# Optimization experiments

Measured on AMD Instinct MI355X. Metric: run time of the kernel, lower is better.

Reference implementation:

```python
import jax, jax.numpy as jnp
import numpy as np

D_IN = 1024
D_OUT = 1024
SEQ = 4096


def setup_inputs() -> dict:
    key = jax.random.key(0)
    kx, kq, kk, kv = jax.random.split(key, 4)
    s = 1.0 / np.sqrt(D_IN)
    return {
        "x": jax.random.normal(kx, (SEQ, D_IN), dtype=jnp.float32),
        # torch Linear weights: shape [d_out, d_in], y = x @ W.T
        "Wq": jax.random.uniform(kq, (D_OUT, D_IN), jnp.float32, -s, s),
        "Wk": jax.random.uniform(kk, (D_OUT, D_IN), jnp.float32, -s, s),
        "Wv": jax.random.uniform(kv, (D_OUT, D_IN), jnp.float32, -s, s),
    }


def reference(x, Wq, Wk, Wv):
    # QKV projections (no bias)
    q = x @ Wq.T  # [N, d_out]
    k = x @ Wk.T
    v = x @ Wv.T
    scale = 1.0 / jnp.sqrt(jnp.asarray(k.shape[-1], x.dtype))
    att = jax.nn.softmax((q @ k.T) * scale, axis=-1)  # [N, N]
    return att @ v  # [N, d_out]
```

## Files before the change

### kernel.cpp

```cpp
#include <hip/hip_runtime.h>
#include <hip/hip_bf16.h>
#include <math.h>

typedef __attribute__((ext_vector_type(8))) short short8;
typedef __attribute__((ext_vector_type(4))) float floatx4;

static __device__ __forceinline__ unsigned short f2bf(float f) {
    union { float f; unsigned int u; } a; a.f = f;
    unsigned int u = a.u;
    return (unsigned short)((u + 0x7FFFu + ((u >> 16) & 1u)) >> 16);
}
static __device__ __forceinline__ float bf2f(unsigned short h) {
    union { unsigned int u; float f; } a; a.u = ((unsigned int)h) << 16;
    return a.f;
}

static __device__ __forceinline__ void cvt8(const float* __restrict__ src,
                                            unsigned short* __restrict__ dst, int i) {
    float4 v0 = *(const float4*)(src + i);
    float4 v1 = *(const float4*)(src + i + 4);
    ushort4 o0, o1;
    o0.x = f2bf(v0.x); o0.y = f2bf(v0.y); o0.z = f2bf(v0.z); o0.w = f2bf(v0.w);
    o1.x = f2bf(v1.x); o1.y = f2bf(v1.y); o1.z = f2bf(v1.z); o1.w = f2bf(v1.w);
    *(ushort4*)(dst + i) = o0;
    *(ushort4*)(dst + i + 4) = o1;
}

struct CV { const float* x; unsigned short* xb;
            const float* W[3]; unsigned short* Wb[3]; float* l; };
__global__ __launch_bounds__(256)
void cvt_all(CV a) {
    int b = blockIdx.x, t = threadIdx.x;
    if (b < 2048) {
        cvt8(a.x, a.xb, (b * 256 + t) * 8);
    } else if (b < 3584) {
        int z  = (b - 2048) >> 9;
        int bb = (b - 2048) & 511;
        cvt8(a.W[z], a.Wb[z], (bb * 256 + t) * 8);
    } else {
        float4 zz = {0.f, 0.f, 0.f, 0.f};
        #pragma unroll
        for (int c = 0; c < 4; c++)
            *(float4*)(a.l + t * 16 + c * 4) = zz;
    }
}

#define DSR(dst, base, OFF)                                                    \
    asm volatile("ds_read_b128 %0, %1 offset:%2"                               \
                 : "=v"(dst) : "v"(base), "n"(OFF))
#define DSR4(arr, base, O)                                                     \
    do { DSR(arr[0], base, (O));        DSR(arr[1], base, (O) + 1024);         \
         DSR(arr[2], base, (O) + 2048); DSR(arr[3], base, (O) + 3072); } while (0)
#define LGKM(N) asm volatile("s_waitcnt lgkmcnt(" #N ")" ::: "memory")
#define SBAR()  asm volatile("s_barrier" ::: "memory")
#define SB0     __builtin_amdgcn_sched_barrier(0)

typedef __attribute__((address_space(3))) char* lds3p;

__device__ __forceinline__ void gemm256_core(
    const unsigned short* __restrict__ A, const unsigned short* __restrict__ B,
    int lda, int k_begin, int bm, int bn,
    unsigned short* lds, floatx4 (&acc)[8][4])
{
    const int t    = threadIdx.x;
    const int wave = t >> 6;
    const int lane = t & 63;
    const int wrow = wave >> 2;
    const int wcol = wave & 3;
    const int lm   = lane & 15;
    const int ce8  = (((lane >> 4) ^ ((lm >> 1) & 3)) << 3);

    const int srow = t >> 2;
    const int gsh  = (((t & 3) ^ ((srow >> 1) & 3)) << 3);
    const unsigned short* srcA = A + (size_t)(bm + srow) * lda + k_begin + gsh;
    const unsigned short* srcB = B + (size_t)(bn + srow) * lda + k_begin + gsh;
    const size_t rstep = (size_t)128 * lda;
    char* ldsc = (char*)lds;
    const int w1k = wave << 10;

    lds3p lp3 = (lds3p)lds;
    lds3p va = lp3 + (((wrow << 7) + lm) * 64 + (ce8 << 1));
    lds3p vb = lp3 + (65536 + ((wcol << 6) + lm) * 64 + (ce8 << 1));

#define STAGE(kind, kh, tau) do {                                              \
        int taue_ = (tau) >= 16 ? (tau) - 2 : (tau);   \
        int ko_ = (taue_ << 6) + ((kh) << 5);                                  \
        unsigned lo_ = ((kind) << 16) + (((tau) & 1) << 15) + ((kh) << 14) + w1k; \
        const unsigned short* s_ = ((kind) ? srcB : srcA) + ko_;               \
        __builtin_amdgcn_global_load_lds(                                      \
            (const __attribute__((address_space(1))) void*)s_,                 \
            (__attribute__((address_space(3))) void*)(ldsc + lo_), 16, 0, 0);  \
        __builtin_amdgcn_global_load_lds(                                      \
            (const __attribute__((address_space(1))) void*)(s_ + rstep),       \
            (__attribute__((address_space(3))) void*)(ldsc + lo_ + 8192), 16, 0, 0); \
    } while (0)

#define MF1(R, AV, BV)                                                         \
    do {                                                                       \
        acc[R][0] = __builtin_amdgcn_mfma_f32_16x16x32_bf16(AV, BV[0], acc[R][0], 0, 0, 0); \
        acc[R][1] = __builtin_amdgcn_mfma_f32_16x16x32_bf16(AV, BV[1], acc[R][1], 0, 0, 0); \
        acc[R][2] = __builtin_amdgcn_mfma_f32_16x16x32_bf16(AV, BV[2], acc[R][2], 0, 0, 0); \
        acc[R][3] = __builtin_amdgcn_mfma_f32_16x16x32_bf16(AV, BV[3], acc[R][3], 0, 0, 0); \
    } while (0)
#define MFMAG(R0, NA, BV)                                                      \
    do { MF1((R0) + 0, NA[0], BV); MF1((R0) + 1, NA[1], BV);                   \
         MF1((R0) + 2, NA[2], BV); MF1((R0) + 3, NA[3], BV); } while (0)

    STAGE(1, 0, 0); STAGE(0, 0, 0); STAGE(1, 1, 0); STAGE(0, 1, 0);
    STAGE(1, 0, 1); STAGE(0, 0, 1); STAGE(1, 1, 1);
    asm volatile("s_waitcnt vmcnt(6)" ::: "memory");
    SBAR();

    constexpr int DB = 32768, KH = 16384;
    short8 naA[4], naB[4], bA[4], bB[4];
    DSR4(naA, va, 0);
    DSR4(bA,  vb, 0);

#define FOURPH(PBc, PBn, TC)                                                   \
                         \
    DSR4(naB, va, (PBc) + 4096);                                               \
    STAGE(0, 1, (TC) + 1);                                                     \
    SBAR(); LGKM(4); SB0;                                                      \
    __builtin_amdgcn_s_setprio(1);                                             \
    MFMAG(0, naA, bA); SB0;                                                    \
    __builtin_amdgcn_s_setprio(0);                                             \
    SBAR();                                                                    \
         \
    DSR4(naA, va, (PBc) + KH);                                                 \
    DSR4(bB,  vb, (PBc) + KH);                                                 \
    STAGE(1, 0, (TC) + 2);                                                     \
    SBAR(); LGKM(8); SB0;                                                      \
    __builtin_amdgcn_s_setprio(1);                                             \
    MFMAG(4, naB, bA); SB0;                                                    \
    __builtin_amdgcn_s_setprio(0);                                             \
    SBAR();                                                                    \
                         \
    DSR4(naB, va, (PBc) + KH + 4096);                                          \
    STAGE(0, 0, (TC) + 2);                                                     \
    SBAR(); LGKM(4); SB0;                                                      \
    __builtin_amdgcn_s_setprio(1);                                             \
    MFMAG(0, naA, bB); SB0;                                                    \
    __builtin_amdgcn_s_setprio(0);                                             \
    SBAR();                                                                    \
     \
    asm volatile("s_waitcnt vmcnt(4)" ::: "memory");                           \
    STAGE(1, 1, (TC) + 2);                                                     \
    SBAR();                                                                    \
    DSR4(naA, va, (PBn));                                                      \
    DSR4(bA,  vb, (PBn));                                                      \
    LGKM(8); SB0;                                                              \
    __builtin_amdgcn_s_setprio(1);                                             \
    MFMAG(4, naB, bB); SB0;                                                    \
    __builtin_amdgcn_s_setprio(0);                                             \
    SBAR();

    for (int t2 = 0; t2 < 16; t2 += 2) {
        FOURPH(0, DB, t2);
        FOURPH(DB, 0, t2 + 1);
    }
    LGKM(0);
#undef FOURPH
#undef STAGE
#undef MFMAG
#undef MF1
}

__device__ __forceinline__ void tile_store256(unsigned short* sm,
                                              floatx4 (&acc)[8][4], float scale, int trans,
                                              unsigned short* __restrict__ C, int ldc,
                                              int rbase, int cbase)
{
    const int t = threadIdx.x, wave = t >> 6, lane = t & 63;
    const int wrow = wave >> 2, wcol = wave & 3;
    const int lm = lane & 15, rq = ((lane >> 4) << 2);
    #pragma unroll
    for (int h = 0; h < 2; h++) {
        __syncthreads();
        if (!trans) {
            if (wrow == h) {
                #pragma unroll
                for (int i = 0; i < 8; i++)
                    #pragma unroll
                    for (int j = 0; j < 4; j++)
                        #pragma unroll
                        for (int r = 0; r < 4; r++)
                            sm[(i * 16 + rq + r) * 264 + wcol * 64 + j * 16 + lm] =
                                f2bf(acc[i][j][r] * scale);
            }
        } else {
            if ((wcol >> 1) == h) {
                #pragma unroll
                for (int i = 0; i < 8; i++)
                    #pragma unroll
                    for (int j = 0; j < 4; j++) {
                        ushort4 v;
                        v.x = f2bf(acc[i][j][0] * scale);
                        v.y = f2bf(acc[i][j][1] * scale);
                        v.z = f2bf(acc[i][j][2] * scale);
                        v.w = f2bf(acc[i][j][3] * scale);
                        *(ushort4*)&sm[((wcol & 1) * 64 + j * 16 + lm) * 264 +
                                       wrow * 128 + i * 16 + rq] = v;
                    }
            }
        }
        __syncthreads();
        #pragma unroll
        for (int p = 0; p < 4; p++) {
            int row = p * 32 + (t >> 4);
            int c0  = (t & 15) * 8;
            *(short8*)&C[(size_t)(rbase + h * 128 + row) * ldc + cbase + c0] =
                *(const short8*)&sm[row * 264 + c0];
            *(short8*)&C[(size_t)(rbase + h * 128 + row) * ldc + cbase + c0 + 128] =
                *(const short8*)&sm[row * 264 + c0 + 128];
        }
    }
}

struct P3 { const unsigned short* W[3]; unsigned short* O[3]; };
__global__ __launch_bounds__(512, 2)
void proj3(const unsigned short* __restrict__ xb, P3 a) {
    __shared__ __align__(16) unsigned short lds[65536];
    const int lid = blockIdx.x;
    const int xcd = lid & 7, rem = lid >> 3;
    const int z   = rem >> 3;
    const int idx = xcd * 8 + (rem & 7);
    const int by = idx >> 2, bx = idx & 3;
    const int bm = by * 256, bn = bx * 256;

    floatx4 acc[8][4];
    #pragma unroll
    for (int i = 0; i < 8; i++)
        #pragma unroll
        for (int j = 0; j < 4; j++) { floatx4 zz = {0.f,0.f,0.f,0.f}; acc[i][j] = zz; }

    gemm256_core(xb, a.W[z], 1024, 0, bm, bn, lds, acc);

    const int trans = (z == 2);
    const float scale = (z == 0) ? 0.03125f : 1.0f;
    tile_store256(lds, acc, scale, trans, a.O[z],
                  trans ? 4096 : 1024, trans ? bn : bm, trans ? bm : bn);
}

__global__ __launch_bounds__(512, 2)
void gemm_ps(const unsigned short* __restrict__ q, const unsigned short* __restrict__ k,
             unsigned short* __restrict__ Pm, float* __restrict__ l) {
    __shared__ __align__(16) unsigned short lds[65536];
    const int lid = blockIdx.x;
    const int xcd = lid & 7, r32 = lid >> 3;
    const int by = ((xcd >> 1) << 2) + (r32 & 3);
    const int bx = ((xcd & 1) << 3) + (r32 >> 2);
    const int bm = by * 256, bn = bx * 256;

    floatx4 acc[8][4];
    #pragma unroll
    for (int i = 0; i < 8; i++)
        #pragma unroll
        for (int j = 0; j < 4; j++) { floatx4 zz = {0.f,0.f,0.f,0.f}; acc[i][j] = zz; }

    gemm256_core(q, k, 1024, 0, bm, bn, lds, acc);

    const int lane = threadIdx.x & 63, wave = threadIdx.x >> 6;
    const int wrow = wave >> 2;
    const int lm = lane & 15, rq = ((lane >> 4) << 2);
    #pragma unroll
    for (int i = 0; i < 8; i++) {
        #pragma unroll
        for (int r = 0; r < 4; r++) {
            float rs = 0.f;
            #pragma unroll
            for (int j = 0; j < 4; j++) {
                float e = __expf(acc[i][j][r]);
                acc[i][j][r] = e;
                rs += e;
            }
            rs += __shfl_xor(rs, 1);
            rs += __shfl_xor(rs, 2);
            rs += __shfl_xor(rs, 4);
            rs += __shfl_xor(rs, 8);
            if (lm == 0) atomicAdd(l + bm + wrow * 128 + i * 16 + rq + r, rs);
        }
    }
    tile_store256(lds, acc, 1.0f, 0, Pm, 4096, bm, bn);
}

__global__ __launch_bounds__(512, 2)
void gemm_osplit(const unsigned short* __restrict__ Pm, const unsigned short* __restrict__ vT,
                 unsigned short* __restrict__ Opart) {
    __shared__ __align__(16) unsigned short lds[65536];
    const int lid = blockIdx.x;
    const int xcd = lid & 7, r32 = lid >> 3;
    const int z   = r32 & 3;
    const int idx = (r32 >> 2) * 8 + xcd;
    const int by = idx >> 2, bx = idx & 3;

    floatx4 acc[8][4];
    #pragma unroll
    for (int i = 0; i < 8; i++)
        #pragma unroll
        for (int j = 0; j < 4; j++) { floatx4 zz = {0.f,0.f,0.f,0.f}; acc[i][j] = zz; }

    gemm256_core(Pm, vT, 4096, z * 1024, by * 256, bx * 256, lds, acc);

    tile_store256(lds, acc, 1.0f, 0, Opart + (size_t)z * (4096 * 1024), 1024,
                  by * 256, bx * 256);
}

__global__ __launch_bounds__(256)
void reduce_scale(const unsigned short* __restrict__ Op, const float* __restrict__ l,
                  float* __restrict__ out) {
    int i = (blockIdx.x * 256 + threadIdx.x) * 4;
    ushort4 a = *(const ushort4*)(Op + i);
    ushort4 b = *(const ushort4*)(Op + 4194304 + i);
    ushort4 c = *(const ushort4*)(Op + 8388608 + i);
    ushort4 d = *(const ushort4*)(Op + 12582912 + i);
    float inv = 1.0f / l[i >> 10];
    float4 o;
    o.x = (bf2f(a.x) + bf2f(b.x) + bf2f(c.x) + bf2f(d.x)) * inv;
    o.y = (bf2f(a.y) + bf2f(b.y) + bf2f(c.y) + bf2f(d.y)) * inv;
    o.z = (bf2f(a.z) + bf2f(b.z) + bf2f(c.z) + bf2f(d.z)) * inv;
    o.w = (bf2f(a.w) + bf2f(b.w) + bf2f(c.w) + bf2f(d.w)) * inv;
    *(float4*)(out + i) = o;
}

extern "C" void kernel_launch(void* const* d_in, const int* in_sizes, int n_in,
                              void* d_out, int out_size, void* d_ws, size_t ws_size,
                              hipStream_t stream) {
    const float* x  = (const float*)d_in[0];
    const float* Wq = (const float*)d_in[1];
    const float* Wk = (const float*)d_in[2];
    const float* Wv = (const float*)d_in[3];
    float* out = (float*)d_out;

    char* ws = (char*)d_ws;
    const size_t MB = 1u << 20;
    unsigned short* vTb = (unsigned short*)(ws);
    unsigned short* xb  = (unsigned short*)(ws + 8 * MB);
    unsigned short* Wqb = (unsigned short*)(ws + 16 * MB);
    unsigned short* Wkb = (unsigned short*)(ws + 18 * MB);
    unsigned short* Wvb = (unsigned short*)(ws + 20 * MB);
    unsigned short* qb  = (unsigned short*)(ws + 22 * MB);
    unsigned short* kb  = (unsigned short*)(ws + 30 * MB);
    unsigned short* P   = (unsigned short*)(ws + 40 * MB);
    float*          l   = (float*)(ws + 72 * MB);
    unsigned short* Opart = (unsigned short*)(ws + 8 * MB);

    dim3 b256(256), b512(512);
    CV cv = {x, xb, {Wq, Wk, Wv}, {Wqb, Wkb, Wvb}, l};
    cvt_all<<<dim3(3585), b256, 0, stream>>>(cv);

    P3 p3 = {{Wqb, Wkb, Wvb}, {qb, kb, vTb}};
    proj3<<<dim3(192), b512, 0, stream>>>(xb, p3);

    gemm_ps<<<dim3(256), b512, 0, stream>>>(qb, kb, P, l);

    gemm_osplit<<<dim3(256), b512, 0, stream>>>(P, vTb, Opart);

    reduce_scale<<<dim3(4096), b256, 0, stream>>>(Opart, l, out);
}
```

Measured before the change: 197.0 us.

## Reschedule GEMM main loop: issue LDS reads after MFMA, wait on vmcnt per phase

Restructures the four-phase software pipeline in the 256x256 GEMM core. LDS fragment reads for the next phase are now issued after each MFMA group instead of before it, and every phase waits with vmcnt(6)/lgkmcnt(0) rather than using partial lgkm counts and a single vmcnt(4). The staging order of the global-to-LDS loads is also changed. The aim is to hide ds_read latency behind the MFMAs and simplify the wait schedule, at the cost of stricter waits per phase that may stall the pipeline or leave ordering hazards on LDS buffers.

```diff
diff --git a/kernel.cpp b/kernel.cpp
--- a/kernel.cpp
+++ b/kernel.cpp
@@ -52,6 +52,7 @@
     do { DSR(arr[0], base, (O));        DSR(arr[1], base, (O) + 1024);         \
          DSR(arr[2], base, (O) + 2048); DSR(arr[3], base, (O) + 3072); } while (0)
 #define LGKM(N) asm volatile("s_waitcnt lgkmcnt(" #N ")" ::: "memory")
+#define VMC6()  asm volatile("s_waitcnt vmcnt(6)" ::: "memory")
 #define SBAR()  asm volatile("s_barrier" ::: "memory")
 #define SB0     __builtin_amdgcn_sched_barrier(0)
 
@@ -107,51 +108,49 @@
          MF1((R0) + 2, NA[2], BV); MF1((R0) + 3, NA[3], BV); } while (0)
 
     STAGE(1, 0, 0); STAGE(0, 0, 0); STAGE(1, 1, 0); STAGE(0, 1, 0);
-    STAGE(1, 0, 1); STAGE(0, 0, 1); STAGE(1, 1, 1);
-    asm volatile("s_waitcnt vmcnt(6)" ::: "memory");
+    STAGE(1, 0, 1); STAGE(1, 1, 1); STAGE(0, 0, 1);
+    VMC6();
     SBAR();
 
     constexpr int DB = 32768, KH = 16384;
-    short8 naA[4], naB[4], bA[4], bB[4];
-    DSR4(naA, va, 0);
-    DSR4(bA,  vb, 0);
+    short8 na_cur[4], na_nxt[4], b_cur[4], b_nxt[4];
+    DSR4(na_cur, va, 0);
+    DSR4(b_cur,  vb, 0);
 
 #define FOURPH(PBc, PBn, TC)                                                   \
-                         \
-    DSR4(naB, va, (PBc) + 4096);                                               \
+                                              \
     STAGE(0, 1, (TC) + 1);                                                     \
-    SBAR(); LGKM(4); SB0;                                                      \
+    VMC6(); LGKM(0); SB0;                                                      \
     __builtin_amdgcn_s_setprio(1);                                             \
-    MFMAG(0, naA, bA); SB0;                                                    \
+    MFMAG(0, na_cur, b_cur); SB0;                                              \
     __builtin_amdgcn_s_setprio(0);                                             \
+    DSR4(na_nxt, va, (PBc) + 4096);                   \
     SBAR();                                                                    \
-         \
-    DSR4(naA, va, (PBc) + KH);                                                 \
-    DSR4(bB,  vb, (PBc) + KH);                                                 \
+                                              \
     STAGE(1, 0, (TC) + 2);                                                     \
-    SBAR(); LGKM(8); SB0;                                                      \
+    VMC6(); LGKM(0); SB0;                                                      \
     __builtin_amdgcn_s_setprio(1);                                             \
-    MFMAG(4, naB, bA); SB0;                                                    \
+    MFMAG(4, na_nxt, b_cur); SB0;                                              \
     __builtin_amdgcn_s_setprio(0);                                             \
+    DSR4(na_cur, va, (PBc) + KH);                     \
+    DSR4(b_nxt,  vb, (PBc) + KH);                      \
     SBAR();                                                                    \
-                         \
-    DSR4(naB, va, (PBc) + KH + 4096);                                          \
+                                              \
+    STAGE(1, 1, (TC) + 2);                                                     \
+    VMC6(); LGKM(0); SB0;                                                      \
+    __builtin_amdgcn_s_setprio(1);                                             \
+    MFMAG(0, na_cur, b_nxt); SB0;                                              \
+    __builtin_amdgcn_s_setprio(0);                                             \
+    DSR4(na_nxt, va, (PBc) + KH + 4096);              \
+    SBAR();                                                                    \
+                                              \
     STAGE(0, 0, (TC) + 2);                                                     \
-    SBAR(); LGKM(4); SB0;                                                      \
+    VMC6(); LGKM(0); SB0;                                                      \
     __builtin_amdgcn_s_setprio(1);                                             \
-    MFMAG(0, naA, bB); SB0;                                                    \
+    MFMAG(4, na_nxt, b_nxt); SB0;                                              \
     __builtin_amdgcn_s_setprio(0);                                             \
-    SBAR();                                                                    \
-     \
-    asm volatile("s_waitcnt vmcnt(4)" ::: "memory");                           \
-    STAGE(1, 1, (TC) + 2);                                                     \
-    SBAR();                                                                    \
-    DSR4(naA, va, (PBn));                                                      \
-    DSR4(bA,  vb, (PBn));                                                      \
-    LGKM(8); SB0;                                                              \
-    __builtin_amdgcn_s_setprio(1);                                             \
-    MFMAG(4, naB, bB); SB0;                                                    \
-    __builtin_amdgcn_s_setprio(0);                                             \
+    DSR4(na_cur, va, (PBn));                     \
+    DSR4(b_cur,  vb, (PBn));                                     \
     SBAR();
 
     for (int t2 = 0; t2 < 16; t2 += 2) {
```

Result: no change. 195.4 us, median of 3 (-0.9%).
